# Kernel tuning notes

Measured on AMD Instinct MI355X. Metric: run time of the kernel, lower is better.

The kernel has to match this reference:

```python
import jax, jax.numpy as jnp
import numpy as np

IN_F, N_ASS, OUT_F = 256, 4096, 256
P_CONNECT = 0.05
BATCH = 128


def _build_graph(in_f, n_ass, out_f, p, seed=0):
    """Replicates Random_RNN.random_graph_init edge structure (numpy, deterministic)."""
    rng = np.random.default_rng(seed)
    ass0 = in_f
    out0 = in_f + n_ass
    total = out0 + out_f
    # input -> associative edges, each input guaranteed >=1 outgoing edge
    m1 = rng.random((in_f, n_ass)) < p
    for i in np.where(~m1.any(axis=1))[0]:
        m1[i, rng.integers(n_ass)] = True
    in_src, in_dst = np.nonzero(m1)
    in_dst = in_dst + ass0
    # associative -> (associative | output) edges, each assoc >=1 outgoing edge
    m2 = rng.random((n_ass, n_ass + out_f)) < p
    for i in np.where(~m2.any(axis=1))[0]:
        m2[i, rng.integers(n_ass + out_f)] = True
    a_src, a_dst = np.nonzero(m2)
    a_src = a_src + ass0
    a_dst = a_dst + ass0
    # every output neuron guaranteed >=1 incoming edge from an associative neuron
    no_in = np.where(~m2[:, n_ass:].any(axis=0))[0]
    if no_in.size:
        a_src = np.concatenate([a_src, ass0 + rng.integers(0, n_ass, size=no_in.size)])
        a_dst = np.concatenate([a_dst, out0 + no_in])
    return (in_src.astype(np.int32), in_dst.astype(np.int32),
            a_src.astype(np.int32), a_dst.astype(np.int32), total)


def setup_inputs() -> dict:
    key = jax.random.key(0)
    k_x, k_wi, k_wa = jax.random.split(key, 3)
    in_src, in_dst, ass_src, ass_dst, total = _build_graph(IN_F, N_ASS, OUT_F, P_CONNECT)
    x = jax.random.normal(k_x, (BATCH, IN_F), dtype=jnp.float32)
    input_weights = jax.random.normal(k_wi, (in_src.shape[0],), dtype=jnp.float32) * 0.05
    associative_weights = jax.random.normal(k_wa, (ass_src.shape[0],), dtype=jnp.float32) * 0.05
    return {
        "x": x,
        "input_weights": input_weights,
        "associative_weights": associative_weights,
        "in_src": jnp.asarray(in_src),
        "in_dst": jnp.asarray(in_dst),
        "ass_src": jnp.asarray(ass_src),
        "ass_dst": jnp.asarray(ass_dst),
        "total_neurons": int(total),
        "out_features": OUT_F,
    }


def reference(x, input_weights, associative_weights, in_src, in_dst, ass_src, ass_dst,
              total_neurons, out_features):
    # Hop 1: input neurons emit x along their edges to associative neurons.
    # msg1: [E_in, B] = gather of input activations scaled by per-edge weight.
    msg1 = x.T[in_src] * input_weights[:, None]
    acc = jax.ops.segment_sum(msg1, in_dst, num_segments=total_neurons)  # [N, B]
    # Hop 2: associative neurons propagate along their edges (to assoc + output).
    msg2 = acc[ass_src] * associative_weights[:, None]  # [E_ass, B]
    acc2 = jax.ops.segment_sum(msg2, ass_dst, num_segments=total_neurons)  # [N, B]
    # Read activations of output neurons (last out_features node indices).
    return acc2[total_neurons - out_features:].T  # [B, out_features]
```

## Files before the change

kernel.cpp:

```cpp
#include <hip/hip_runtime.h>

#define IN_F   256
#define N_ASS  4096
#define OUT_F  256
#define BATCH  128
#define ASS0   256
#define OUT0   4352
#define SPLITK1 2
#define SPLITK2 32

#define OFF_W2T (1024 * 1024)
#define OFF_P1  (2 * 1024 * 1024)
#define OFF_P2  (4 * 1024 * 1024)

__global__ __launch_bounds__(256) void scatter_kernel(
        const int* __restrict__ src1, const int* __restrict__ dst1,
        const float* __restrict__ w1, int E1,
        const int* __restrict__ src2, const int* __restrict__ dst2,
        const float* __restrict__ w2, int E2,
        float* __restrict__ W1T, float* __restrict__ W2T) {
    const int e = blockIdx.x * 256 + threadIdx.x;
    if (e < E1) {
        W1T[src1[e] * N_ASS + (dst1[e] - ASS0)] = w1[e];
    } else if (e - E1 < E2) {
        const int i = e - E1;
        const int d = dst2[i];
        if (d >= OUT0)
            W2T[(src2[i] - ASS0) * OUT_F + (d - OUT0)] = w2[i];
    }
}

template<int N_, bool DUAL_A>
__global__ __launch_bounds__(256) void gemm32(const float* __restrict__ A, int lda,
                                              const float* __restrict__ B,
                                              float* __restrict__ P) {
    __shared__ __align__(16) float As[32][68];
    __shared__ __align__(16) float Bs[64][68];

    const int tid = threadIdx.x;
    const int m0 = blockIdx.x * 32;
    const int n0 = blockIdx.y * 64;
    const int z  = blockIdx.z;
    const int kBeg = z * 128;

    float4 areg[2], breg[4];
    #pragma unroll
    for (int r = 0; r < 2; ++r) {
        const int j = tid + r * 256;
        const float* ap = A + (size_t)(m0 + (j >> 4)) * lda + kBeg + (j & 15) * 4;
        areg[r] = *(const float4*)ap;
        if constexpr (DUAL_A) {
            const float4 a2 = *(const float4*)(ap + (size_t)BATCH * lda);
            areg[r].x += a2.x; areg[r].y += a2.y; areg[r].z += a2.z; areg[r].w += a2.w;
        }
    }
    #pragma unroll
    for (int r = 0; r < 4; ++r) {
        const int j = tid + r * 256;
        breg[r] = *(const float4*)(B + (size_t)(kBeg + (j >> 4)) * N_ + n0 + (j & 15) * 4);
    }

    const int ty2 = (tid >> 4) * 2;
    const int tx4 = (tid & 15) * 4;
    float c[2][4] = {};

    #pragma unroll
    for (int it = 0; it < 2; ++it) {
        if (it) __syncthreads();
        #pragma unroll
        for (int r = 0; r < 2; ++r) {
            const int j = tid + r * 256;
            *(float4*)&As[j >> 4][(j & 15) * 4] = areg[r];
        }
        #pragma unroll
        for (int r = 0; r < 4; ++r) {
            const int j = tid + r * 256;
            *(float4*)&Bs[j >> 4][(j & 15) * 4] = breg[r];
        }
        __syncthreads();
        if (it == 0) {
            const int k0 = kBeg + 64;
            #pragma unroll
            for (int r = 0; r < 2; ++r) {
                const int j = tid + r * 256;
                const float* ap = A + (size_t)(m0 + (j >> 4)) * lda + k0 + (j & 15) * 4;
                areg[r] = *(const float4*)ap;
                if constexpr (DUAL_A) {
                    const float4 a2 = *(const float4*)(ap + (size_t)BATCH * lda);
                    areg[r].x += a2.x; areg[r].y += a2.y; areg[r].z += a2.z; areg[r].w += a2.w;
                }
            }
            #pragma unroll
            for (int r = 0; r < 4; ++r) {
                const int j = tid + r * 256;
                breg[r] = *(const float4*)(B + (size_t)(k0 + (j >> 4)) * N_ + n0 + (j & 15) * 4);
            }
        }
        #pragma unroll
        for (int kk = 0; kk < 64; kk += 4) {
            const float4 a0 = *(const float4*)&As[ty2][kk];
            const float4 a1 = *(const float4*)&As[ty2 + 1][kk];
            #pragma unroll
            for (int u = 0; u < 4; ++u) {
                const float4 b = *(const float4*)&Bs[kk + u][tx4];
                const float a0u = ((const float*)&a0)[u];
                const float a1u = ((const float*)&a1)[u];
                c[0][0] = fmaf(a0u, b.x, c[0][0]); c[0][1] = fmaf(a0u, b.y, c[0][1]);
                c[0][2] = fmaf(a0u, b.z, c[0][2]); c[0][3] = fmaf(a0u, b.w, c[0][3]);
                c[1][0] = fmaf(a1u, b.x, c[1][0]); c[1][1] = fmaf(a1u, b.y, c[1][1]);
                c[1][2] = fmaf(a1u, b.z, c[1][2]); c[1][3] = fmaf(a1u, b.w, c[1][3]);
            }
        }
    }

    float* Pz = P + (size_t)z * (BATCH * N_);
    #pragma unroll
    for (int i = 0; i < 2; ++i)
        *(float4*)&Pz[(size_t)(m0 + ty2 + i) * N_ + n0 + tx4] =
            make_float4(c[i][0], c[i][1], c[i][2], c[i][3]);
}

__global__ __launch_bounds__(128) void reduce_kernel(const float4* __restrict__ P4,
                                                     float4* __restrict__ out4) {
    const int g = blockIdx.x * 128 + threadIdx.x;
    float4 s = make_float4(0.f, 0.f, 0.f, 0.f);
    #pragma unroll
    for (int z = 0; z < SPLITK2; ++z) {
        const float4 p = P4[(size_t)z * 8192 + g];
        s.x += p.x; s.y += p.y; s.z += p.z; s.w += p.w;
    }
    out4[g] = s;
}

extern "C" void kernel_launch(void* const* d_in, const int* in_sizes, int n_in,
                              void* d_out, int out_size, void* d_ws, size_t ws_size,
                              hipStream_t stream) {
    const float* x      = (const float*)d_in[0];
    const float* w_in   = (const float*)d_in[1];
    const float* w_ass  = (const float*)d_in[2];
    const int*   in_src = (const int*)d_in[3];
    const int*   in_dst = (const int*)d_in[4];
    const int*   a_src  = (const int*)d_in[5];
    const int*   a_dst  = (const int*)d_in[6];
    const int E1 = in_sizes[3];
    const int E2 = in_sizes[5];

    float* ws  = (float*)d_ws;
    float* W1T = ws;
    float* W2T = ws + OFF_W2T;
    float* P1  = ws + OFF_P1;
    float* P2  = ws + OFF_P2;

    scatter_kernel<<<(E1 + E2 + 255) / 256, 256, 0, stream>>>(
        in_src, in_dst, w_in, E1, a_src, a_dst, w_ass, E2, W1T, W2T);

    gemm32<N_ASS, false><<<dim3(4, 64, SPLITK1), 256, 0, stream>>>(x, IN_F, W1T, P1);

    gemm32<OUT_F, true><<<dim3(4, 4, SPLITK2), 256, 0, stream>>>(P1, N_ASS, W2T, P2);

    reduce_kernel<<<64, 128, 0, stream>>>((const float4*)P2, (float4*)d_out);
}
```

Baseline: 36.56 us.

## Overlap second-layer weight scatter with first GEMM in a combined launch

The combined scatter kernel is split in two. The input-edge scatter runs alone, and the associative-edge scatter (about 880K edges) now shares one launch with the first GEMM: block indices below 512 do GEMM tiles and the remaining 1024 blocks grid-stride over the edges. This takes the large associative-edge scatter off the critical path before GEMM1, so it overlaps with GEMM compute. It adds a branchy heterogeneous kernel whose shared-memory footprint also applies to the scatter blocks, which could limit occupancy.

```diff
diff --git a/kernel.cpp b/kernel.cpp
--- a/kernel.cpp
+++ b/kernel.cpp
@@ -8,39 +8,28 @@
 #define OUT0   4352
 #define SPLITK1 2
 #define SPLITK2 32
+#define G1_BLOCKS 512
+#define SC_BLOCKS 1024
 
 #define OFF_W2T (1024 * 1024)
 #define OFF_P1  (2 * 1024 * 1024)
 #define OFF_P2  (4 * 1024 * 1024)
 
-__global__ __launch_bounds__(256) void scatter_kernel(
-        const int* __restrict__ src1, const int* __restrict__ dst1,
-        const float* __restrict__ w1, int E1,
-        const int* __restrict__ src2, const int* __restrict__ dst2,
-        const float* __restrict__ w2, int E2,
-        float* __restrict__ W1T, float* __restrict__ W2T) {
+__global__ __launch_bounds__(256) void scatter1_kernel(
+        const int* __restrict__ src, const int* __restrict__ dst,
+        const float* __restrict__ w, int E1, float* __restrict__ W1T) {
     const int e = blockIdx.x * 256 + threadIdx.x;
-    if (e < E1) {
-        W1T[src1[e] * N_ASS + (dst1[e] - ASS0)] = w1[e];
-    } else if (e - E1 < E2) {
-        const int i = e - E1;
-        const int d = dst2[i];
-        if (d >= OUT0)
-            W2T[(src2[i] - ASS0) * OUT_F + (d - OUT0)] = w2[i];
-    }
+    if (e < E1)
+        W1T[src[e] * N_ASS + (dst[e] - ASS0)] = w[e];
 }
 
 template<int N_, bool DUAL_A>
-__global__ __launch_bounds__(256) void gemm32(const float* __restrict__ A, int lda,
-                                              const float* __restrict__ B,
-                                              float* __restrict__ P) {
-    __shared__ __align__(16) float As[32][68];
-    __shared__ __align__(16) float Bs[64][68];
-
+__device__ __forceinline__ void gemm32_body(const float* __restrict__ A, int lda,
+                                            const float* __restrict__ B,
+                                            float* __restrict__ P,
+                                            int m0, int n0, int z,
+                                            float (*As)[68], float (*Bs)[68]) {
     const int tid = threadIdx.x;
-    const int m0 = blockIdx.x * 32;
-    const int n0 = blockIdx.y * 64;
-    const int z  = blockIdx.z;
     const int kBeg = z * 128;
 
     float4 areg[2], breg[4];
@@ -120,6 +109,37 @@
             make_float4(c[i][0], c[i][1], c[i][2], c[i][3]);
 }
 
+__global__ __launch_bounds__(256) void g1_plus_scatter2(
+        const float* __restrict__ x, const float* __restrict__ W1T,
+        float* __restrict__ P1,
+        const int* __restrict__ a_src, const int* __restrict__ a_dst,
+        const float* __restrict__ w_ass, int E2, float* __restrict__ W2T) {
+    const int bid = blockIdx.x;
+    if (bid < G1_BLOCKS) {
+        __shared__ __align__(16) float As[32][68];
+        __shared__ __align__(16) float Bs[64][68];
+        gemm32_body<N_ASS, false>(x, IN_F, W1T, P1,
+                                  (bid & 3) * 32, ((bid >> 2) & 63) * 64, bid >> 8,
+                                  As, Bs);
+    } else {
+        const int tid = threadIdx.x;
+        for (int e = (bid - G1_BLOCKS) * 256 + tid; e < E2; e += SC_BLOCKS * 256) {
+            const int d = a_dst[e];
+            if (d >= OUT0)
+                W2T[(a_src[e] - ASS0) * OUT_F + (d - OUT0)] = w_ass[e];
+        }
+    }
+}
+
+__global__ __launch_bounds__(256) void gemm2_kernel(const float* __restrict__ P1,
+                                                    const float* __restrict__ W2T,
+                                                    float* __restrict__ P2) {
+    __shared__ __align__(16) float As[32][68];
+    __shared__ __align__(16) float Bs[64][68];
+    gemm32_body<OUT_F, true>(P1, N_ASS, W2T, P2,
+                             blockIdx.x * 32, blockIdx.y * 64, blockIdx.z, As, Bs);
+}
+
 __global__ __launch_bounds__(128) void reduce_kernel(const float4* __restrict__ P4,
                                                      float4* __restrict__ out4) {
     const int g = blockIdx.x * 128 + threadIdx.x;
@@ -151,12 +171,12 @@
     float* P1  = ws + OFF_P1;
     float* P2  = ws + OFF_P2;
 
-    scatter_kernel<<<(E1 + E2 + 255) / 256, 256, 0, stream>>>(
-        in_src, in_dst, w_in, E1, a_src, a_dst, w_ass, E2, W1T, W2T);
+    scatter1_kernel<<<(E1 + 255) / 256, 256, 0, stream>>>(in_src, in_dst, w_in, E1, W1T);
 
-    gemm32<N_ASS, false><<<dim3(4, 64, SPLITK1), 256, 0, stream>>>(x, IN_F, W1T, P1);
+    g1_plus_scatter2<<<G1_BLOCKS + SC_BLOCKS, 256, 0, stream>>>(
+        x, W1T, P1, a_src, a_dst, w_ass, E2, W2T);
 
-    gemm32<OUT_F, true><<<dim3(4, 4, SPLITK2), 256, 0, stream>>>(P1, N_ASS, W2T, P2);
+    gemm2_kernel<<<dim3(4, 4, SPLITK2), 256, 0, stream>>>(P1, W2T, P2);
 
     reduce_kernel<<<64, 128, 0, stream>>>((const float4*)P2, (float4*)d_out);
 }
```

Result: no change. 36.45 us (-0.3%).
